# Kernel tuning notes

Hardware: AMD Instinct MI355X
Metric: run time of the kernel (lower is better)

Reference implementation:

```python
import jax, jax.numpy as jnp
import numpy as np

N_NODES = 100000
N_EDGES = 640000
NUM_GRAPHS = 128
NUM_FEATURES = 128
HIDDEN = 16
NUM_CLASSES = 10


def setup_inputs() -> dict:
    key = jax.random.key(0)
    ks = jax.random.split(key, 9)
    x = jax.random.normal(ks[0], (N_NODES, NUM_FEATURES), dtype=jnp.float32)
    edge_index = jax.random.randint(ks[1], (2, N_EDGES), 0, N_NODES, dtype=jnp.int64)
    batch = jnp.sort(jax.random.randint(ks[2], (N_NODES,), 0, NUM_GRAPHS, dtype=jnp.int64))
    W1 = jax.random.normal(ks[3], (NUM_FEATURES, HIDDEN), dtype=jnp.float32) * 0.1
    b1 = jax.random.normal(ks[4], (HIDDEN,), dtype=jnp.float32) * 0.1
    W2 = jax.random.normal(ks[5], (HIDDEN, HIDDEN), dtype=jnp.float32) * 0.1
    b2 = jax.random.normal(ks[6], (HIDDEN,), dtype=jnp.float32) * 0.1
    Wfc = jax.random.normal(ks[7], (HIDDEN, NUM_CLASSES), dtype=jnp.float32) * 0.1
    bfc = jax.random.normal(ks[8], (NUM_CLASSES,), dtype=jnp.float32) * 0.1
    return {"x": x, "edge_index": edge_index, "batch": batch,
            "W1": W1, "b1": b1, "W2": W2, "b2": b2, "Wfc": Wfc, "bfc": bfc}


def reference(x, edge_index, batch, W1, b1, W2, b2, Wfc, bfc):
    src, dst = edge_index[0], edge_index[1]

    def gin_layer(h, W, b):
        # GINConv (eps=0): nn((1+eps)*x_i + sum_{j in N(i)} x_j)
        agg = jax.ops.segment_sum(h[src], dst, num_segments=N_NODES)
        return jax.nn.relu((h + agg) @ W + b)

    h = gin_layer(x, W1, b1)   # [N, 16]
    h = gin_layer(h, W2, b2)   # [N, 16]

    # global mean pool over graphs
    sums = jax.ops.segment_sum(h, batch, num_segments=NUM_GRAPHS)        # [G, 16]
    counts = jax.ops.segment_sum(jnp.ones((N_NODES,), h.dtype), batch,
                                 num_segments=NUM_GRAPHS)                # [G]
    pooled = sums / jnp.maximum(counts, 1.0)[:, None]
    return pooled @ Wfc + bfc  # [G, num_classes]
```

## Files before the change

kernel.cpp:

```cpp
#include <hip/hip_runtime.h>
#include <hip/hip_bf16.h>

#define N_NODES   100000
#define N_EDGES   640000
#define NUM_GRAPHS 128
#define NUM_FEAT  128
#define HIDDEN    16
#define NUM_CLS   10

#define NBLK   256
#define EPB    (N_EDGES / NBLK)
#define NBUCK  256
#define BSHIFT 9
#define BNODES 512

#define MM1_ROWS 64
__global__ __launch_bounds__(256) void k_mm1_bcount(const float* __restrict__ x,
                                                    const float* __restrict__ W1,
                                                    float* __restrict__ y,
                                                    const int* __restrict__ ei,
                                                    int* __restrict__ cnt,
                                                    int N, int gridMM1) {
    __shared__ float sx[MM1_ROWS][132];
    __shared__ float sw[NUM_FEAT * HIDDEN];
    const int t = threadIdx.x;

    if (blockIdx.x >= gridMM1) {
        int* h = (int*)&sx[0][0];
        const int b = blockIdx.x - gridMM1;
        h[t] = 0;
        __syncthreads();
        const int e0 = b * EPB, e1 = e0 + EPB;
        for (int e = e0 + t; e < e1; e += 256)
            atomicAdd(&h[ei[N_EDGES + e] >> BSHIFT], 1);
        __syncthreads();
        cnt[t * NBLK + b] = h[t];
        return;
    }

    const int rowbase = blockIdx.x * MM1_ROWS;
    const int nrows = min(MM1_ROWS, N - rowbase);

    for (int i = t; i < NUM_FEAT * HIDDEN; i += 256) sw[i] = W1[i];

    for (int i = t; i < nrows * 32; i += 256) {
        int r = i >> 5, q = i & 31;
        float4 v = ((const float4*)(x + (size_t)(rowbase + r) * NUM_FEAT))[q];
        *(float4*)&sx[r][q * 4] = v;
    }
    __syncthreads();

    const int r  = t >> 2;
    const int c0 = (t & 3) * 4;
    if (r < nrows) {
        float4 o = {0.f, 0.f, 0.f, 0.f};
        #pragma unroll 4
        for (int k4 = 0; k4 < 32; ++k4) {
            float4 xv = *(const float4*)&sx[r][k4 * 4];
            const float* wb = &sw[(k4 * 4) * HIDDEN + c0];
            float4 w0 = *(const float4*)(wb);
            float4 w1 = *(const float4*)(wb + HIDDEN);
            float4 w2 = *(const float4*)(wb + 2 * HIDDEN);
            float4 w3 = *(const float4*)(wb + 3 * HIDDEN);
            o.x += xv.x * w0.x + xv.y * w1.x + xv.z * w2.x + xv.w * w3.x;
            o.y += xv.x * w0.y + xv.y * w1.y + xv.z * w2.y + xv.w * w3.y;
            o.z += xv.x * w0.z + xv.y * w1.z + xv.z * w2.z + xv.w * w3.z;
            o.w += xv.x * w0.w + xv.y * w1.w + xv.z * w2.w + xv.w * w3.w;
        }
        ((float4*)(y + (size_t)(rowbase + r) * HIDDEN))[t & 3] = o;
    }
}

__global__ __launch_bounds__(256) void k_bscan(int* __restrict__ cnt,
                                               int* __restrict__ btot,
                                               float* __restrict__ sums) {
    __shared__ int s[256];
    const int k = blockIdx.x, t = threadIdx.x;
    if (k == 0) {
        for (int i = t; i < NUM_GRAPHS * HIDDEN + NUM_GRAPHS; i += 256) sums[i] = 0.f;
    }
    int v = cnt[k * NBLK + t];
    s[t] = v;
    __syncthreads();
    for (int off = 1; off < 256; off <<= 1) {
        int add = (t >= off) ? s[t - off] : 0;
        __syncthreads();
        s[t] += add;
        __syncthreads();
    }
    cnt[k * NBLK + t] = s[t] - v;
    if (t == 255) btot[k] = s[t];
}

__global__ __launch_bounds__(256) void k_place(const int* __restrict__ ei,
                                               const int* __restrict__ cnt,
                                               const int* __restrict__ btot,
                                               unsigned* __restrict__ packed) {
    __shared__ int bb[NBUCK];
    __shared__ int cur[NBUCK];
    const int t = threadIdx.x, b = blockIdx.x;
    int v = btot[t];
    bb[t] = v;
    __syncthreads();
    for (int off = 1; off < 256; off <<= 1) {
        int add = (t >= off) ? bb[t - off] : 0;
        __syncthreads();
        bb[t] += add;
        __syncthreads();
    }
    cur[t] = (bb[t] - v) + cnt[t * NBLK + b];
    __syncthreads();
    const int e0 = b * EPB, e1 = e0 + EPB;
    for (int e = e0 + t; e < e1; e += 256) {
        int srcv = ei[e];
        int dstv = ei[N_EDGES + e];
        int k = dstv >> BSHIFT;
        int slot = atomicAdd(&cur[k], 1);
        packed[slot] = ((unsigned)(dstv & (BNODES - 1)) << 17) | (unsigned)srcv;
    }
}

__global__ __launch_bounds__(256) void k_build(const unsigned* __restrict__ packed,
                                               const int* __restrict__ btot,
                                               int* __restrict__ row,
                                               int* __restrict__ srcidx) {
    __shared__ int bb[NBUCK];
    __shared__ int h[BNODES];
    __shared__ int ps[256];
    __shared__ int e2[BNODES];
    __shared__ int cur[BNODES];
    const int k = blockIdx.x, t = threadIdx.x;

    int v = btot[t];
    bb[t] = v;
    __syncthreads();
    for (int off = 1; off < 256; off <<= 1) {
        int add = (t >= off) ? bb[t - off] : 0;
        __syncthreads();
        bb[t] += add;
        __syncthreads();
    }
    __syncthreads();
    const int s1 = bb[k];
    const int s0 = s1 - btot[k];

    h[t] = 0; h[t + 256] = 0;
    __syncthreads();
    for (int i = s0 + t; i < s1; i += 256)
        atomicAdd(&h[packed[i] >> 17], 1);
    __syncthreads();
    int pv = h[2 * t] + h[2 * t + 1];
    ps[t] = pv;
    __syncthreads();
    for (int off = 1; off < 256; off <<= 1) {
        int add = (t >= off) ? ps[t - off] : 0;
        __syncthreads();
        ps[t] += add;
        __syncthreads();
    }
    int ex = ps[t] - pv;
    e2[2 * t] = ex;               e2[2 * t + 1] = ex + h[2 * t];
    cur[2 * t] = ex;              cur[2 * t + 1] = ex + h[2 * t];
    __syncthreads();
    #pragma unroll
    for (int jj = 0; jj < 2; ++jj) {
        int j = t + jj * 256;
        int node = (k << BSHIFT) + j;
        if (node <= N_NODES) row[node] = s0 + e2[j];
    }
    __syncthreads();
    for (int i = s0 + t; i < s1; i += 256) {
        unsigned p = packed[i];
        int dl = p >> 17;
        int slot = atomicAdd(&cur[dl], 1);
        srcidx[s0 + slot] = (int)(p & 0x1FFFFu);
    }
}

__global__ __launch_bounds__(256) void k_g1f(const int* __restrict__ row,
                                             const int* __restrict__ srcidx,
                                             const float* __restrict__ A,
                                             const float* __restrict__ bias,
                                             const float* __restrict__ W2,
                                             float* __restrict__ B, int N) {
    __shared__ float sw[HIDDEN * HIDDEN];
    const int t = threadIdx.x;
    if (t < HIDDEN * HIDDEN) sw[t] = W2[t];
    __syncthreads();
    const int n = blockIdx.x * 64 + (t >> 2);
    const int p = t & 3;
    if (n >= N) return;
    const int r0 = row[n];
    const int d  = row[n + 1] - r0;
    float4 acc = ((const float4*)(A + (size_t)n * HIDDEN))[p];
    for (int i = 0; i < d; ++i) {
        int s = srcidx[r0 + i];
        float4 v = ((const float4*)(A + (size_t)s * HIDDEN))[p];
        acc.x += v.x; acc.y += v.y; acc.z += v.z; acc.w += v.w;
    }
    const float4 bv = ((const float4*)bias)[p];
    acc.x = fmaxf(acc.x + bv.x, 0.f);
    acc.y = fmaxf(acc.y + bv.y, 0.f);
    acc.z = fmaxf(acc.z + bv.z, 0.f);
    acc.w = fmaxf(acc.w + bv.w, 0.f);
    const int lane = t & 63;
    const int qbase = lane & ~3;
    const int c0 = p * 4;
    float4 o = {0.f, 0.f, 0.f, 0.f};
    #pragma unroll
    for (int q = 0; q < 4; ++q) {
        float hx = __shfl(acc.x, qbase + q, 64);
        float hy = __shfl(acc.y, qbase + q, 64);
        float hz = __shfl(acc.z, qbase + q, 64);
        float hw = __shfl(acc.w, qbase + q, 64);
        const float* wb = &sw[(q * 4) * HIDDEN + c0];
        float4 w0 = *(const float4*)(wb);
        float4 w1 = *(const float4*)(wb + HIDDEN);
        float4 w2 = *(const float4*)(wb + 2 * HIDDEN);
        float4 w3 = *(const float4*)(wb + 3 * HIDDEN);
        o.x += hx * w0.x + hy * w1.x + hz * w2.x + hw * w3.x;
        o.y += hx * w0.y + hy * w1.y + hz * w2.y + hw * w3.y;
        o.z += hx * w0.z + hy * w1.z + hz * w2.z + hw * w3.z;
        o.w += hx * w0.w + hy * w1.w + hz * w2.w + hw * w3.w;
    }
    ((float4*)(B + (size_t)n * HIDDEN))[p] = o;
}

#define POOL_BLOCKS 1024
__global__ __launch_bounds__(256) void k_g2p(const int* __restrict__ row,
                                             const int* __restrict__ srcidx,
                                             const float* __restrict__ B,
                                             const float* __restrict__ bias,
                                             const int* __restrict__ batch,
                                             float* __restrict__ sums,
                                             float* __restrict__ counts,
                                             int N, int chunk) {
    __shared__ float ssum[NUM_GRAPHS * HIDDEN];
    __shared__ float scnt[NUM_GRAPHS];
    const int t = threadIdx.x;
    for (int i = t; i < NUM_GRAPHS * HIDDEN; i += 256) ssum[i] = 0.f;
    if (t < NUM_GRAPHS) scnt[t] = 0.f;
    __syncthreads();

    const int n0 = blockIdx.x * chunk;
    const int n1 = min(n0 + chunk, N);
    const int lane = t & 63;
    const int p = t & 3;
    const float4 bv = ((const float4*)bias)[p];

    for (int nb = n0; nb < n1; nb += 64) {
        int n = nb + (t >> 2);
        bool active = (n < n1);
        int nc = active ? n : (n1 - 1);
        int g = batch[nc];
        float4 h = {0.f, 0.f, 0.f, 0.f};
        if (active) {
            int r0 = row[n];
            int d  = row[n + 1] - r0;
            h = ((const float4*)(B + (size_t)n * HIDDEN))[p];
            for (int i = 0; i < d; ++i) {
                int s = srcidx[r0 + i];
                float4 v = ((const float4*)(B + (size_t)s * HIDDEN))[p];
                h.x += v.x; h.y += v.y; h.z += v.z; h.w += v.w;
            }
            h.x = fmaxf(h.x + bv.x, 0.f);
            h.y = fmaxf(h.y + bv.y, 0.f);
            h.z = fmaxf(h.z + bv.z, 0.f);
            h.w = fmaxf(h.w + bv.w, 0.f);
        }
        int gf = __builtin_amdgcn_readfirstlane(g);
        bool uniform = (__ballot(g == gf) == ~0ull);
        if (uniform) {
            #pragma unroll
            for (int m = 4; m <= 32; m <<= 1) {
                h.x += __shfl_xor(h.x, m, 64);
                h.y += __shfl_xor(h.y, m, 64);
                h.z += __shfl_xor(h.z, m, 64);
                h.w += __shfl_xor(h.w, m, 64);
            }
            if (lane < 4) {
                float* sp = &ssum[gf * HIDDEN + p * 4];
                atomicAdd(sp + 0, h.x);
                atomicAdd(sp + 1, h.y);
                atomicAdd(sp + 2, h.z);
                atomicAdd(sp + 3, h.w);
            }
            if (lane == 0) {
                int wfirst = nb + ((t >> 6) << 4);
                int cnt = min(16, n1 - wfirst);
                if (cnt > 0) atomicAdd(&scnt[gf], (float)cnt);
            }
        } else if (active) {
            float* sp = &ssum[g * HIDDEN + p * 4];
            atomicAdd(sp + 0, h.x);
            atomicAdd(sp + 1, h.y);
            atomicAdd(sp + 2, h.z);
            atomicAdd(sp + 3, h.w);
            if (p == 0) atomicAdd(&scnt[g], 1.f);
        }
    }
    __syncthreads();
    for (int i = t; i < NUM_GRAPHS * HIDDEN; i += 256) {
        float v = ssum[i];
        if (v != 0.f) atomicAdd(&sums[i], v);
    }
    if (t < NUM_GRAPHS) {
        float v = scnt[t];
        if (v != 0.f) atomicAdd(&counts[t], v);
    }
}

__global__ __launch_bounds__(256) void k_fc(const float* __restrict__ sums,
                                            const float* __restrict__ counts,
                                            const float* __restrict__ Wfc,
                                            const float* __restrict__ bfc,
                                            float* __restrict__ out) {
    int t = blockIdx.x * 256 + threadIdx.x;
    if (t >= NUM_GRAPHS * NUM_CLS) return;
    int g = t / NUM_CLS, c = t % NUM_CLS;
    float inv = 1.0f / fmaxf(counts[g], 1.0f);
    float acc = bfc[c];
    #pragma unroll
    for (int k = 0; k < HIDDEN; ++k)
        acc += (sums[g * HIDDEN + k] * inv) * Wfc[k * NUM_CLS + c];
    out[t] = acc;
}

extern "C" void kernel_launch(void* const* d_in, const int* in_sizes, int n_in,
                              void* d_out, int out_size, void* d_ws, size_t ws_size,
                              hipStream_t stream) {
    const float* x    = (const float*)d_in[0];
    const int*   ei   = (const int*)d_in[1];
    const int*   batch= (const int*)d_in[2];
    const float* W1   = (const float*)d_in[3];
    const float* b1   = (const float*)d_in[4];
    const float* W2   = (const float*)d_in[5];
    const float* b2   = (const float*)d_in[6];
    const float* Wfc  = (const float*)d_in[7];
    const float* bfc  = (const float*)d_in[8];
    float* out = (float*)d_out;

    const size_t NB = (size_t)N_NODES * HIDDEN * sizeof(float);
    char* ws = (char*)d_ws;
    size_t off = 0;
    float* A      = (float*)(ws + off); off += NB;
    float* B      = (float*)(ws + off); off += NB;
    float* sums   = (float*)(ws + off); off += (size_t)NUM_GRAPHS * HIDDEN * sizeof(float);
    float* counts = (float*)(ws + off); off += (size_t)NUM_GRAPHS * sizeof(float);
    int* row    = (int*)(ws + off); off += (size_t)(N_NODES + 4) * sizeof(int);
    int* cnt    = (int*)(ws + off); off += (size_t)NBUCK * NBLK * sizeof(int);
    int* btot   = (int*)(ws + off); off += (size_t)NBUCK * sizeof(int);
    off = (off + 15) & ~(size_t)15;
    int* srcidx = (int*)(ws + off); off += (size_t)N_EDGES * sizeof(int);
    unsigned* packed = (unsigned*)B;

    const int gridMM1 = (N_NODES + MM1_ROWS - 1) / MM1_ROWS;
    const int gridG1  = (N_NODES + 63) / 64;
    const int poolChunk = (N_NODES + POOL_BLOCKS - 1) / POOL_BLOCKS;

    k_mm1_bcount<<<gridMM1 + NBLK, 256, 0, stream>>>(x, W1, A, ei, cnt,
                                                     N_NODES, gridMM1);
    k_bscan<<<NBUCK, 256, 0, stream>>>(cnt, btot, sums);
    k_place<<<NBLK, 256, 0, stream>>>(ei, cnt, btot, packed);
    k_build<<<NBUCK, 256, 0, stream>>>(packed, btot, row, srcidx);

    k_g1f<<<gridG1, 256, 0, stream>>>(row, srcidx, A, b1, W2, B, N_NODES);

    k_g2p<<<POOL_BLOCKS, 256, 0, stream>>>(row, srcidx, B, b2, batch, sums, counts,
                                           N_NODES, poolChunk);
    k_fc<<<(NUM_GRAPHS * NUM_CLS + 255) / 256, 256, 0, stream>>>(sums, counts, Wfc, bfc, out);
}
```

Measured before the change: 84.72 us.

## Fold bucket scan into placement and fuse final FC into pooling kernel

Removes the separate bucket-scan kernel: each placement block now recomputes per-bucket totals and its own prefix by reading the transposed count matrix, then scans bucket totals locally and publishes bucket bases for the build kernel. The final FC kernel is folded into the pooling kernel using a last-block-done atomic counter, and the zeroing of sums, counts and the counter moves into the placement kernel. This cuts two kernel launches and their serialization gaps, at the cost of every placement block reading the full 256x256 count matrix and relying on a threadfence-based completion pattern.

New measurement: 103.3 us. +21.9%, slower.

```diff
diff --git a/kernel.cpp b/kernel.cpp
--- a/kernel.cpp
+++ b/kernel.cpp
@@ -34,7 +34,7 @@
         for (int e = e0 + t; e < e1; e += 256)
             atomicAdd(&h[ei[N_EDGES + e] >> BSHIFT], 1);
         __syncthreads();
-        cnt[t * NBLK + b] = h[t];
+        cnt[b * NBUCK + t] = h[t];
         return;
     }
 
@@ -71,45 +71,38 @@
     }
 }
 
-__global__ __launch_bounds__(256) void k_bscan(int* __restrict__ cnt,
-                                               int* __restrict__ btot,
-                                               float* __restrict__ sums) {
-    __shared__ int s[256];
-    const int k = blockIdx.x, t = threadIdx.x;
-    if (k == 0) {
-        for (int i = t; i < NUM_GRAPHS * HIDDEN + NUM_GRAPHS; i += 256) sums[i] = 0.f;
-    }
-    int v = cnt[k * NBLK + t];
-    s[t] = v;
-    __syncthreads();
-    for (int off = 1; off < 256; off <<= 1) {
-        int add = (t >= off) ? s[t - off] : 0;
-        __syncthreads();
-        s[t] += add;
-        __syncthreads();
-    }
-    cnt[k * NBLK + t] = s[t] - v;
-    if (t == 255) btot[k] = s[t];
-}
-
 __global__ __launch_bounds__(256) void k_place(const int* __restrict__ ei,
                                                const int* __restrict__ cnt,
-                                               const int* __restrict__ btot,
-                                               unsigned* __restrict__ packed) {
-    __shared__ int bb[NBUCK];
+                                               int* __restrict__ bases,
+                                               unsigned* __restrict__ packed,
+                                               int* __restrict__ zarea, int nz) {
+    __shared__ int s[NBUCK];
     __shared__ int cur[NBUCK];
     const int t = threadIdx.x, b = blockIdx.x;
-    int v = btot[t];
-    bb[t] = v;
-    __syncthreads();
-    for (int off = 1; off < 256; off <<= 1) {
-        int add = (t >= off) ? bb[t - off] : 0;
-        __syncthreads();
-        bb[t] += add;
-        __syncthreads();
-    }
-    cur[t] = (bb[t] - v) + cnt[t * NBLK + b];
-    __syncthreads();
+
+    int tot = 0, own = 0;
+    for (int i = 0; i < NBLK; ++i) {
+        int v = cnt[i * NBUCK + t];
+        tot += v;
+        own += (i < b) ? v : 0;
+    }
+    s[t] = tot;
+    __syncthreads();
+    for (int off = 1; off < NBUCK; off <<= 1) {
+        int add = (t >= off) ? s[t - off] : 0;
+        __syncthreads();
+        s[t] += add;
+        __syncthreads();
+    }
+    const int base = s[t] - tot;
+    cur[t] = base + own;
+    if (b == 0) {
+        bases[t] = base;
+        if (t == NBUCK - 1) bases[NBUCK] = N_EDGES;
+        for (int i = t; i < nz; i += 256) zarea[i] = 0;
+    }
+    __syncthreads();
+
     const int e0 = b * EPB, e1 = e0 + EPB;
     for (int e = e0 + t; e < e1; e += 256) {
         int srcv = ei[e];
@@ -121,28 +114,16 @@
 }
 
 __global__ __launch_bounds__(256) void k_build(const unsigned* __restrict__ packed,
-                                               const int* __restrict__ btot,
+                                               const int* __restrict__ bases,
                                                int* __restrict__ row,
                                                int* __restrict__ srcidx) {
-    __shared__ int bb[NBUCK];
     __shared__ int h[BNODES];
     __shared__ int ps[256];
     __shared__ int e2[BNODES];
     __shared__ int cur[BNODES];
     const int k = blockIdx.x, t = threadIdx.x;
-
-    int v = btot[t];
-    bb[t] = v;
-    __syncthreads();
-    for (int off = 1; off < 256; off <<= 1) {
-        int add = (t >= off) ? bb[t - off] : 0;
-        __syncthreads();
-        bb[t] += add;
-        __syncthreads();
-    }
-    __syncthreads();
-    const int s1 = bb[k];
-    const int s0 = s1 - btot[k];
+    const int s0 = bases[k];
+    const int s1 = bases[k + 1];
 
     h[t] = 0; h[t + 256] = 0;
     __syncthreads();
@@ -234,9 +215,14 @@
                                              const int* __restrict__ batch,
                                              float* __restrict__ sums,
                                              float* __restrict__ counts,
+                                             unsigned* __restrict__ done,
+                                             const float* __restrict__ Wfc,
+                                             const float* __restrict__ bfc,
+                                             float* __restrict__ out,
                                              int N, int chunk) {
     __shared__ float ssum[NUM_GRAPHS * HIDDEN];
     __shared__ float scnt[NUM_GRAPHS];
+    __shared__ unsigned sdone;
     const int t = threadIdx.x;
     for (int i = t; i < NUM_GRAPHS * HIDDEN; i += 256) ssum[i] = 0.f;
     if (t < NUM_GRAPHS) scnt[t] = 0.f;
@@ -308,22 +294,21 @@
         float v = scnt[t];
         if (v != 0.f) atomicAdd(&counts[t], v);
     }
-}
-
-__global__ __launch_bounds__(256) void k_fc(const float* __restrict__ sums,
-                                            const float* __restrict__ counts,
-                                            const float* __restrict__ Wfc,
-                                            const float* __restrict__ bfc,
-                                            float* __restrict__ out) {
-    int t = blockIdx.x * 256 + threadIdx.x;
-    if (t >= NUM_GRAPHS * NUM_CLS) return;
-    int g = t / NUM_CLS, c = t % NUM_CLS;
-    float inv = 1.0f / fmaxf(counts[g], 1.0f);
-    float acc = bfc[c];
-    #pragma unroll
-    for (int k = 0; k < HIDDEN; ++k)
-        acc += (sums[g * HIDDEN + k] * inv) * Wfc[k * NUM_CLS + c];
-    out[t] = acc;
+    __syncthreads();
+    if (t == 0) sdone = atomicAdd(done, 1u);
+    __syncthreads();
+    if (sdone == POOL_BLOCKS - 1) {
+        __threadfence();
+        for (int i = t; i < NUM_GRAPHS * NUM_CLS; i += 256) {
+            int g = i / NUM_CLS, c = i % NUM_CLS;
+            float inv = 1.0f / fmaxf(counts[g], 1.0f);
+            float acc = bfc[c];
+            #pragma unroll
+            for (int kk = 0; kk < HIDDEN; ++kk)
+                acc += (sums[g * HIDDEN + kk] * inv) * Wfc[kk * NUM_CLS + c];
+            out[i] = acc;
+        }
+    }
 }
 
 extern "C" void kernel_launch(void* const* d_in, const int* in_sizes, int n_in,
@@ -345,11 +330,13 @@
     size_t off = 0;
     float* A      = (float*)(ws + off); off += NB;
     float* B      = (float*)(ws + off); off += NB;
-    float* sums   = (float*)(ws + off); off += (size_t)NUM_GRAPHS * HIDDEN * sizeof(float);
-    float* counts = (float*)(ws + off); off += (size_t)NUM_GRAPHS * sizeof(float);
+    float*    sums   = (float*)(ws + off); off += (size_t)NUM_GRAPHS * HIDDEN * sizeof(float);
+    float*    counts = (float*)(ws + off); off += (size_t)NUM_GRAPHS * sizeof(float);
+    unsigned* done   = (unsigned*)(ws + off); off += 16;
+    const int nz = NUM_GRAPHS * HIDDEN + NUM_GRAPHS + 1;
     int* row    = (int*)(ws + off); off += (size_t)(N_NODES + 4) * sizeof(int);
-    int* cnt    = (int*)(ws + off); off += (size_t)NBUCK * NBLK * sizeof(int);
-    int* btot   = (int*)(ws + off); off += (size_t)NBUCK * sizeof(int);
+    int* cnt    = (int*)(ws + off); off += (size_t)NBLK * NBUCK * sizeof(int);
+    int* bases  = (int*)(ws + off); off += (size_t)(NBUCK + 1) * sizeof(int);
     off = (off + 15) & ~(size_t)15;
     int* srcidx = (int*)(ws + off); off += (size_t)N_EDGES * sizeof(int);
     unsigned* packed = (unsigned*)B;
@@ -360,13 +347,11 @@
 
     k_mm1_bcount<<<gridMM1 + NBLK, 256, 0, stream>>>(x, W1, A, ei, cnt,
                                                      N_NODES, gridMM1);
-    k_bscan<<<NBUCK, 256, 0, stream>>>(cnt, btot, sums);
-    k_place<<<NBLK, 256, 0, stream>>>(ei, cnt, btot, packed);
-    k_build<<<NBUCK, 256, 0, stream>>>(packed, btot, row, srcidx);
+    k_place<<<NBLK, 256, 0, stream>>>(ei, cnt, bases, packed, (int*)sums, nz);
+    k_build<<<NBUCK, 256, 0, stream>>>(packed, bases, row, srcidx);
 
     k_g1f<<<gridG1, 256, 0, stream>>>(row, srcidx, A, b1, W2, B, N_NODES);
 
     k_g2p<<<POOL_BLOCKS, 256, 0, stream>>>(row, srcidx, B, b2, batch, sums, counts,
-                                           N_NODES, poolChunk);
-    k_fc<<<(NUM_GRAPHS * NUM_CLS + 255) / 256, 256, 0, stream>>>(sums, counts, Wfc, bfc, out);
-}
+                                           done, Wfc, bfc, out, N_NODES, poolChunk);
+}
```

## Store hidden features in fp16 and fuse final FC into pooling kernel

Applied to the files above, without the earlier changes.

Intermediate node feature buffers A and B are now stored as half precision and converted to float on load, so the random per-edge gathers move half as many bytes. The separate FC kernel is removed: the last pooling block to finish, detected through an atomic counter, computes the output, which saves one launch. A done counter is zeroed together with sums and counts. The cost is fp16 rounding of intermediate activations, which may loosen accuracy, plus a small serial tail in the final block.

After: 90.12 us. +6.4%, slower.

```diff
diff --git a/kernel.cpp b/kernel.cpp
--- a/kernel.cpp
+++ b/kernel.cpp
@@ -1,5 +1,5 @@
 #include <hip/hip_runtime.h>
-#include <hip/hip_bf16.h>
+#include <hip/hip_fp16.h>
 
 #define N_NODES   100000
 #define N_EDGES   640000
@@ -15,19 +15,34 @@
 #define BNODES 512
 
 #define MM1_ROWS 64
+#define GRID_MM1 ((N_NODES + MM1_ROWS - 1) / MM1_ROWS)
+
+__device__ __forceinline__ float4 ldh4(const __half* p) {
+    float2 raw = *(const float2*)p;
+    const __half2* h = (const __half2*)&raw;
+    float2 a = __half22float2(h[0]);
+    float2 b = __half22float2(h[1]);
+    return make_float4(a.x, a.y, b.x, b.y);
+}
+__device__ __forceinline__ void sth4(__half* p, float4 v) {
+    float2 raw;
+    ((__half2*)&raw)[0] = __floats2half2_rn(v.x, v.y);
+    ((__half2*)&raw)[1] = __floats2half2_rn(v.z, v.w);
+    *(float2*)p = raw;
+}
+
 __global__ __launch_bounds__(256) void k_mm1_bcount(const float* __restrict__ x,
                                                     const float* __restrict__ W1,
-                                                    float* __restrict__ y,
+                                                    __half* __restrict__ y,
                                                     const int* __restrict__ ei,
-                                                    int* __restrict__ cnt,
-                                                    int N, int gridMM1) {
+                                                    int* __restrict__ cnt) {
     __shared__ float sx[MM1_ROWS][132];
     __shared__ float sw[NUM_FEAT * HIDDEN];
     const int t = threadIdx.x;
 
-    if (blockIdx.x >= gridMM1) {
+    if (blockIdx.x >= GRID_MM1) {
         int* h = (int*)&sx[0][0];
-        const int b = blockIdx.x - gridMM1;
+        const int b = blockIdx.x - GRID_MM1;
         h[t] = 0;
         __syncthreads();
         const int e0 = b * EPB, e1 = e0 + EPB;
@@ -39,10 +54,9 @@
     }
 
     const int rowbase = blockIdx.x * MM1_ROWS;
-    const int nrows = min(MM1_ROWS, N - rowbase);
+    const int nrows = min(MM1_ROWS, N_NODES - rowbase);
 
     for (int i = t; i < NUM_FEAT * HIDDEN; i += 256) sw[i] = W1[i];
-
     for (int i = t; i < nrows * 32; i += 256) {
         int r = i >> 5, q = i & 31;
         float4 v = ((const float4*)(x + (size_t)(rowbase + r) * NUM_FEAT))[q];
@@ -67,17 +81,17 @@
             o.z += xv.x * w0.z + xv.y * w1.z + xv.z * w2.z + xv.w * w3.z;
             o.w += xv.x * w0.w + xv.y * w1.w + xv.z * w2.w + xv.w * w3.w;
         }
-        ((float4*)(y + (size_t)(rowbase + r) * HIDDEN))[t & 3] = o;
+        sth4(y + (size_t)(rowbase + r) * HIDDEN + (t & 3) * 4, o);
     }
 }
 
 __global__ __launch_bounds__(256) void k_bscan(int* __restrict__ cnt,
                                                int* __restrict__ btot,
-                                               float* __restrict__ sums) {
+                                               int* __restrict__ zarea, int nz) {
     __shared__ int s[256];
     const int k = blockIdx.x, t = threadIdx.x;
     if (k == 0) {
-        for (int i = t; i < NUM_GRAPHS * HIDDEN + NUM_GRAPHS; i += 256) sums[i] = 0.f;
+        for (int i = t; i < nz; i += 256) zarea[i] = 0;
     }
     int v = cnt[k * NBLK + t];
     s[t] = v;
@@ -102,7 +116,7 @@
     int v = btot[t];
     bb[t] = v;
     __syncthreads();
-    for (int off = 1; off < 256; off <<= 1) {
+    for (int off = 1; off < NBUCK; off <<= 1) {
         int add = (t >= off) ? bb[t - off] : 0;
         __syncthreads();
         bb[t] += add;
@@ -134,13 +148,12 @@
     int v = btot[t];
     bb[t] = v;
     __syncthreads();
-    for (int off = 1; off < 256; off <<= 1) {
+    for (int off = 1; off < NBUCK; off <<= 1) {
         int add = (t >= off) ? bb[t - off] : 0;
         __syncthreads();
         bb[t] += add;
         __syncthreads();
     }
-    __syncthreads();
     const int s1 = bb[k];
     const int s0 = s1 - btot[k];
 
@@ -179,10 +192,10 @@
 
 __global__ __launch_bounds__(256) void k_g1f(const int* __restrict__ row,
                                              const int* __restrict__ srcidx,
-                                             const float* __restrict__ A,
+                                             const __half* __restrict__ A,
                                              const float* __restrict__ bias,
                                              const float* __restrict__ W2,
-                                             float* __restrict__ B, int N) {
+                                             __half* __restrict__ B, int N) {
     __shared__ float sw[HIDDEN * HIDDEN];
     const int t = threadIdx.x;
     if (t < HIDDEN * HIDDEN) sw[t] = W2[t];
@@ -192,10 +205,10 @@
     if (n >= N) return;
     const int r0 = row[n];
     const int d  = row[n + 1] - r0;
-    float4 acc = ((const float4*)(A + (size_t)n * HIDDEN))[p];
+    float4 acc = ldh4(A + (size_t)n * HIDDEN + p * 4);
     for (int i = 0; i < d; ++i) {
         int s = srcidx[r0 + i];
-        float4 v = ((const float4*)(A + (size_t)s * HIDDEN))[p];
+        float4 v = ldh4(A + (size_t)s * HIDDEN + p * 4);
         acc.x += v.x; acc.y += v.y; acc.z += v.z; acc.w += v.w;
     }
     const float4 bv = ((const float4*)bias)[p];
@@ -223,20 +236,25 @@
         o.z += hx * w0.z + hy * w1.z + hz * w2.z + hw * w3.z;
         o.w += hx * w0.w + hy * w1.w + hz * w2.w + hw * w3.w;
     }
-    ((float4*)(B + (size_t)n * HIDDEN))[p] = o;
+    sth4(B + (size_t)n * HIDDEN + p * 4, o);
 }
 
 #define POOL_BLOCKS 1024
 __global__ __launch_bounds__(256) void k_g2p(const int* __restrict__ row,
                                              const int* __restrict__ srcidx,
-                                             const float* __restrict__ B,
+                                             const __half* __restrict__ B,
                                              const float* __restrict__ bias,
                                              const int* __restrict__ batch,
                                              float* __restrict__ sums,
                                              float* __restrict__ counts,
+                                             unsigned* __restrict__ done,
+                                             const float* __restrict__ Wfc,
+                                             const float* __restrict__ bfc,
+                                             float* __restrict__ out,
                                              int N, int chunk) {
     __shared__ float ssum[NUM_GRAPHS * HIDDEN];
     __shared__ float scnt[NUM_GRAPHS];
+    __shared__ unsigned sdone;
     const int t = threadIdx.x;
     for (int i = t; i < NUM_GRAPHS * HIDDEN; i += 256) ssum[i] = 0.f;
     if (t < NUM_GRAPHS) scnt[t] = 0.f;
@@ -257,10 +275,10 @@
         if (active) {
             int r0 = row[n];
             int d  = row[n + 1] - r0;
-            h = ((const float4*)(B + (size_t)n * HIDDEN))[p];
+            h = ldh4(B + (size_t)n * HIDDEN + p * 4);
             for (int i = 0; i < d; ++i) {
                 int s = srcidx[r0 + i];
-                float4 v = ((const float4*)(B + (size_t)s * HIDDEN))[p];
+                float4 v = ldh4(B + (size_t)s * HIDDEN + p * 4);
                 h.x += v.x; h.y += v.y; h.z += v.z; h.w += v.w;
             }
             h.x = fmaxf(h.x + bv.x, 0.f);
@@ -308,22 +326,21 @@
         float v = scnt[t];
         if (v != 0.f) atomicAdd(&counts[t], v);
     }
-}
-
-__global__ __launch_bounds__(256) void k_fc(const float* __restrict__ sums,
-                                            const float* __restrict__ counts,
-                                            const float* __restrict__ Wfc,
-                                            const float* __restrict__ bfc,
-                                            float* __restrict__ out) {
-    int t = blockIdx.x * 256 + threadIdx.x;
-    if (t >= NUM_GRAPHS * NUM_CLS) return;
-    int g = t / NUM_CLS, c = t % NUM_CLS;
-    float inv = 1.0f / fmaxf(counts[g], 1.0f);
-    float acc = bfc[c];
-    #pragma unroll
-    for (int k = 0; k < HIDDEN; ++k)
-        acc += (sums[g * HIDDEN + k] * inv) * Wfc[k * NUM_CLS + c];
-    out[t] = acc;
+    __syncthreads();
+    if (t == 0) sdone = atomicAdd(done, 1u);
+    __syncthreads();
+    if (sdone == POOL_BLOCKS - 1) {
+        __threadfence();
+        for (int i = t; i < NUM_GRAPHS * NUM_CLS; i += 256) {
+            int g = i / NUM_CLS, c = i % NUM_CLS;
+            float inv = 1.0f / fmaxf(counts[g], 1.0f);
+            float acc = bfc[c];
+            #pragma unroll
+            for (int kk = 0; kk < HIDDEN; ++kk)
+                acc += (sums[g * HIDDEN + kk] * inv) * Wfc[kk * NUM_CLS + c];
+            out[i] = acc;
+        }
+    }
 }
 
 extern "C" void kernel_launch(void* const* d_in, const int* in_sizes, int n_in,
@@ -340,33 +357,30 @@
     const float* bfc  = (const float*)d_in[8];
     float* out = (float*)d_out;
 
-    const size_t NB = (size_t)N_NODES * HIDDEN * sizeof(float);
+    const size_t NB = (size_t)N_NODES * HIDDEN * sizeof(__half);
     char* ws = (char*)d_ws;
     size_t off = 0;
-    float* A      = (float*)(ws + off); off += NB;
-    float* B      = (float*)(ws + off); off += NB;
-    float* sums   = (float*)(ws + off); off += (size_t)NUM_GRAPHS * HIDDEN * sizeof(float);
-    float* counts = (float*)(ws + off); off += (size_t)NUM_GRAPHS * sizeof(float);
-    int* row    = (int*)(ws + off); off += (size_t)(N_NODES + 4) * sizeof(int);
-    int* cnt    = (int*)(ws + off); off += (size_t)NBUCK * NBLK * sizeof(int);
-    int* btot   = (int*)(ws + off); off += (size_t)NBUCK * sizeof(int);
+    __half* A = (__half*)(ws + off); off += NB;
+    __half* B = (__half*)(ws + off); off += NB;
+    float*    sums   = (float*)(ws + off);    off += (size_t)NUM_GRAPHS * HIDDEN * sizeof(float);
+    float*    counts = (float*)(ws + off);    off += (size_t)NUM_GRAPHS * sizeof(float);
+    unsigned* done   = (unsigned*)(ws + off); off += 16;
+    const int nz = NUM_GRAPHS * HIDDEN + NUM_GRAPHS + 4;
+    int* row  = (int*)(ws + off); off += (size_t)(N_NODES + 4) * sizeof(int);
+    int* cnt  = (int*)(ws + off); off += (size_t)NBUCK * NBLK * sizeof(int);
+    int* btot = (int*)(ws + off); off += (size_t)NBUCK * sizeof(int);
     off = (off + 15) & ~(size_t)15;
     int* srcidx = (int*)(ws + off); off += (size_t)N_EDGES * sizeof(int);
     unsigned* packed = (unsigned*)B;
 
-    const int gridMM1 = (N_NODES + MM1_ROWS - 1) / MM1_ROWS;
     const int gridG1  = (N_NODES + 63) / 64;
     const int poolChunk = (N_NODES + POOL_BLOCKS - 1) / POOL_BLOCKS;
 
-    k_mm1_bcount<<<gridMM1 + NBLK, 256, 0, stream>>>(x, W1, A, ei, cnt,
-                                                     N_NODES, gridMM1);
-    k_bscan<<<NBUCK, 256, 0, stream>>>(cnt, btot, sums);
+    k_mm1_bcount<<<GRID_MM1 + NBLK, 256, 0, stream>>>(x, W1, A, ei, cnt);
+    k_bscan<<<NBUCK, 256, 0, stream>>>(cnt, btot, (int*)sums, nz);
     k_place<<<NBLK, 256, 0, stream>>>(ei, cnt, btot, packed);
     k_build<<<NBUCK, 256, 0, stream>>>(packed, btot, row, srcidx);
-
     k_g1f<<<gridG1, 256, 0, stream>>>(row, srcidx, A, b1, W2, B, N_NODES);
-
     k_g2p<<<POOL_BLOCKS, 256, 0, stream>>>(row, srcidx, B, b2, batch, sums, counts,
-                                           N_NODES, poolChunk);
-    k_fc<<<(NUM_GRAPHS * NUM_CLS + 255) / 256, 256, 0, stream>>>(sums, counts, Wfc, bfc, out);
-}
+                                           done, Wfc, bfc, out, N_NODES, poolChunk);
+}
```
